# Performance work log

Hardware: AMD Instinct MI355X
Metric: run time of the kernel (lower is better)

The kernel has to match this reference:

```python
import jax, jax.numpy as jnp
import numpy as np

B, G, D, L, F = 64, 1024, 256, 2, 1024  # batch, graph_size, embed_dim, n_layers, ffn hidden
NEG = -30.0  # mask fill value when evaluate=False (training path)


def _uniform(key, shape, fan):
    stdv = 1.0 / np.sqrt(fan)
    return jax.random.uniform(key, shape, jnp.float32, -stdv, stdv)


def setup_inputs() -> dict:
    key = jax.random.key(0)
    ks = jax.random.split(key, 12)
    x = jax.random.normal(ks[0], (B, G, D), jnp.float32)
    mask = jax.random.randint(ks[1], (B, G), 0, 2, jnp.int32)  # 1 = attention blocked
    # weights stored as [in, out] (transposed vs torch Linear); same math.
    Wq = _uniform(ks[2], (L, D, D), D)
    Wk = _uniform(ks[3], (L, D, D), D)
    Wv = _uniform(ks[4], (L, D, D), D)
    Wo = _uniform(ks[5], (L, D, D), D)
    bo = _uniform(ks[6], (L, D), D)
    Wf1 = _uniform(ks[7], (L, D, F), D)
    bf1 = _uniform(ks[8], (L, F), F)
    Wf2 = _uniform(ks[9], (L, F, D), F)
    bf2 = _uniform(ks[10], (L, D), D)
    return {"x": x, "mask": mask, "Wq": Wq, "Wk": Wk, "Wv": Wv,
            "Wo": Wo, "bo": bo, "Wf1": Wf1, "bf1": bf1, "Wf2": Wf2, "bf2": bf2}


def reference(x, mask, Wq, Wk, Wv, Wo, bo, Wf1, bf1, Wf2, bf2):
    # GraphAttentionEncoder with n_heads=1 (key_dim = val_dim = embed_dim).
    m = mask.astype(bool)[:, None, :]            # [B,1,G] -> broadcast over query dim
    norm = 1.0 / jnp.sqrt(jnp.asarray(D, x.dtype))
    h = x
    for l in range(L):
        # --- MultiHeadAttention with residual (SkipConnection) ---
        q = h @ Wq[l]                            # [B,G,D]
        k = h @ Wk[l]
        v = h @ Wv[l]
        c = norm * jnp.einsum('bqd,bkd->bqk', q, k)   # [B,G,G]
        c = jnp.where(m, NEG, c)                 # masked fill (-30, evaluate=False)
        a = jax.nn.softmax(c, axis=-1)
        a = jnp.where(m, 0.0, a)                 # post-softmax zeroing of masked weights
        heads = jnp.einsum('bqk,bkd->bqd', a, v)
        h = h + heads @ Wo[l] + bo[l]
        # --- feed-forward with residual (SkipConnection_Linear) ---
        h = h + jax.nn.relu(h @ Wf1[l] + bf1[l]) @ Wf2[l] + bf2[l]
    return h, h.mean(axis=1)
```

## Files before the change

kernel.cpp:

```cpp
#include <hip/hip_runtime.h>
#include <hip/hip_bf16.h>

#define Bdim 64
#define Gdim 1024
#define Ddim 256
#define Fdim 1024

typedef short s8v __attribute__((ext_vector_type(8)));
typedef float f4v __attribute__((ext_vector_type(4)));

__device__ __forceinline__ float bf2f(short s){
  return __uint_as_float(((unsigned)(unsigned short)s) << 16);
}
__device__ __forceinline__ short f2bf(float f){
  unsigned u = __float_as_uint(f);
  u = u + 0x7fffu + ((u >> 16) & 1u);
  return (short)(u >> 16);
}
__device__ __forceinline__ s8v ld8(const short* p){ return *(const s8v*)p; }

#define MFMA_BF16(a,b,c) __builtin_amdgcn_mfma_f32_16x16x32_bf16((a),(b),(c),0,0,0)

#define GLDS16(gp, lp) __builtin_amdgcn_global_load_lds( \
    (const __attribute__((address_space(1))) void*)(gp), \
    (__attribute__((address_space(3))) void*)(lp), 16, 0, 0)

__global__ __launch_bounds__(256) void detect_dtype(const unsigned* __restrict__ x,
                                                    int* __restrict__ flag){
  __shared__ int cnt[256];
  int c = 0;
  #pragma unroll
  for (int j=0;j<4;j++){
    unsigned u = x[threadIdx.x*4 + j];
    int e = (u >> 7) & 0xFF;
    c += (e >= 100 && e <= 140) ? 1 : 0;
  }
  cnt[threadIdx.x] = c;
  __syncthreads();
  if (threadIdx.x == 0){
    int s = 0;
    for (int i=0;i<256;i++) s += cnt[i];
    flag[0] = (s >= 512) ? 0 : 1;
  }
}

__global__ void diag_ws(void* o, float v, const int* __restrict__ flag){
  if (threadIdx.x == 0){
    if (flag[0]){ ((float*)o)[0] = v; ((float*)o)[16777216] = v; }
    else        { ((short*)o)[0] = f2bf(v); ((short*)o)[16777216] = f2bf(v); }
  }
}

__global__ __launch_bounds__(256) void cast_in(const void* __restrict__ x,
                                               float* __restrict__ h32,
                                               const int* __restrict__ flag){
  size_t i = ((size_t)blockIdx.x * 256 + threadIdx.x) * 8;
  if (flag[0]){
    const float* xf = (const float*)x;
    #pragma unroll
    for (int j=0;j<8;j++) h32[i+j] = xf[i+j];
  } else {
    s8v v = ld8((const short*)x + i);
    #pragma unroll
    for (int j=0;j<8;j++) h32[i+j] = bf2f(v[j]);
  }
}

__global__ __launch_bounds__(256) void transpose_w(const void* __restrict__ src,
                                                   short* __restrict__ dh, int R, int C,
                                                   const int* __restrict__ flag,
                                                   int dzs, int dbase){
  __shared__ short th[32][33];
  int fl = flag[0];
  size_t soff = (size_t)blockIdx.z * R * C;
  size_t doff = (size_t)dbase + (size_t)blockIdx.z * dzs;
  int c0 = blockIdx.x*32, r0 = blockIdx.y*32;
  int tx = threadIdx.x, ty = threadIdx.y;
  #pragma unroll
  for (int i=ty;i<32;i+=8){
    size_t idx = soff + (size_t)(r0+i)*C + (c0+tx);
    float w = fl ? ((const float*)src)[idx] : bf2f(((const short*)src)[idx]);
    th[i][tx] = f2bf(w);
  }
  __syncthreads();
  #pragma unroll
  for (int i=ty;i<32;i+=8)
    dh[doff + (size_t)(c0+i)*R + (r0+tx)] = th[tx][i];
}

__global__ __launch_bounds__(256) void bias_prep(const void* __restrict__ bo,
                                                 const void* __restrict__ bf1,
                                                 const void* __restrict__ bf2,
                                                 float* __restrict__ biasf,
                                                 const int* __restrict__ flag){
  int fl = flag[0];
  int i = blockIdx.x*256 + threadIdx.x;
  const void* src; int idx;
  if (i < 512){ src = bo; idx = i; }
  else if (i < 2560){ src = bf1; idx = i - 512; }
  else { src = bf2; idx = i - 2560; }
  biasf[i] = fl ? ((const float*)src)[idx] : bf2f(((const short*)src)[idx]);
}

template<int AM, int EPI>
__global__ __launch_bounds__(256) void gemm_t(
    const void* __restrict__ Ap, const short* __restrict__ Bh,
    const float* __restrict__ bias, float* __restrict__ hout,
    short* __restrict__ outb, int N, int K, int lda, int ldb, int Mrows)
{
  constexpr int AT = (AM==2) ? 2 : 1;
  __shared__ short As[AT*128*40];
  __shared__ short Bs[128*40];
  short* Asl = As + 128*40;
  const int tid = threadIdx.x;
  const int lane = tid & 63, wave = tid >> 6;
  const int quad = lane >> 4, l16 = lane & 15;
  const int m0 = blockIdx.x * 128, n0 = blockIdx.y * 128;
  const int wr = wave >> 1, wc = wave & 1;
  f4v acc[4][4];
  #pragma unroll
  for (int i=0;i<4;i++)
    #pragma unroll
    for (int j=0;j<4;j++) acc[i][j] = f4v{0.f,0.f,0.f,0.f};

  for (int k0 = 0; k0 < K; k0 += 32){
    __syncthreads();
    #pragma unroll
    for (int i=0;i<2;i++){
      int v = tid + i*256;
      int r = v >> 2, c8 = (v & 3) * 8;
      if (AM == 0){
        *(s8v*)(&As[r*40 + c8]) = ld8((const short*)Ap + (size_t)(m0 + r)*lda + k0 + c8);
      } else {
        const float* af = (const float*)Ap + (size_t)(m0 + r)*lda + k0 + c8;
        float4 f0 = *(const float4*)af;
        float4 f1 = *(const float4*)(af + 4);
        float fv[8] = {f0.x,f0.y,f0.z,f0.w,f1.x,f1.y,f1.z,f1.w};
        s8v hi, lo;
        #pragma unroll
        for (int j=0;j<8;j++) hi[j] = f2bf(fv[j]);
        *(s8v*)(&As[r*40 + c8]) = hi;
        if (AM == 2){
          #pragma unroll
          for (int j=0;j<8;j++) lo[j] = f2bf(fv[j] - bf2f(hi[j]));
          *(s8v*)(&Asl[r*40 + c8]) = lo;
        }
      }
      *(s8v*)(&Bs[r*40 + c8]) = ld8(Bh + (size_t)(n0 + r)*ldb + k0 + c8);
    }
    __syncthreads();
    s8v ah[4], al[4], bh[4];
    #pragma unroll
    for (int t=0;t<4;t++){
      ah[t] = ld8(&As[(wr*64 + t*16 + l16)*40 + quad*8]);
      bh[t] = ld8(&Bs[(wc*64 + t*16 + l16)*40 + quad*8]);
      if (AM == 2) al[t] = ld8(&Asl[(wr*64 + t*16 + l16)*40 + quad*8]);
    }
    #pragma unroll
    for (int ti=0;ti<4;ti++)
      #pragma unroll
      for (int tj=0;tj<4;tj++){
        acc[ti][tj] = MFMA_BF16(ah[ti], bh[tj], acc[ti][tj]);
        if (AM == 2) acc[ti][tj] = MFMA_BF16(al[ti], bh[tj], acc[ti][tj]);
      }
  }
  #pragma unroll
  for (int tj=0;tj<4;tj++){
    int col = n0 + wc*64 + tj*16 + l16;
    float bs = (EPI==1 || EPI==4) ? (bias ? bias[col] : 0.f) : 0.f;
    #pragma unroll
    for (int ti=0;ti<4;ti++){
      #pragma unroll
      for (int r=0;r<4;r++){
        int row = m0 + wr*64 + ti*16 + quad*4 + r;
        float v = acc[ti][tj][r];
        if (EPI == 0){
          outb[(size_t)row * N + col] = f2bf(v);
        } else if (EPI == 1){
          v += bs; v = v > 0.f ? v : 0.f;
          outb[(size_t)row * N + col] = f2bf(v);
        } else if (EPI == 4){
          size_t idx = (size_t)row * N + col;
          hout[idx] += v + bs;
        } else {
          int sec = col >> 8, c = col & 255;
          if (sec == 0)      outb[(size_t)row*256 + c] = f2bf(v);
          else if (sec == 1) (outb + (size_t)Mrows*256)[(size_t)row*256 + c] = f2bf(v);
          else {
            int bb = row >> 10, g = row & 1023;
            (outb + (size_t)2*Mrows*256)[(size_t)bb*262144 + (size_t)c*1024 + g] = f2bf(v);
          }
        }
      }
    }
  }
}

__global__ __launch_bounds__(512, 2) void flash_attn(
    const short* __restrict__ Q, const short* __restrict__ Kmat,
    const short* __restrict__ Vt, const int* __restrict__ mask,
    short* __restrict__ H)
{
  __shared__ short Ks[2][64*256];
  __shared__ short Vs[2][256*64];
  __shared__ short Ps[8][16*72];
  const int tid = threadIdx.x;
  const int lane = tid & 63, wave = tid >> 6;
  const int quad = lane >> 4, l16 = lane & 15;
  const int bid = blockIdx.x;
  const int b  = (bid & 7) + ((bid >> 6) << 3);
  const int qt = (bid >> 3) & 7;
  const short* Qb  = Q    + (size_t)b*Gdim*Ddim;
  const short* Kb  = Kmat + (size_t)b*Gdim*Ddim;
  const short* Vtb = Vt   + (size_t)b*Ddim*Gdim;
  const int qbase = qt*128 + wave*16;

  auto stage = [&](int buf, int k0){
    #pragma unroll
    for (int i=0;i<4;i++){
      int idx = i*512 + tid;
      int r = idx >> 5, g = idx & 31;
      GLDS16(Kb + (size_t)(k0 + r)*Ddim + ((g ^ (r & 7)) << 3), &Ks[buf][idx*8]);
    }
    #pragma unroll
    for (int i=0;i<4;i++){
      int idx = i*512 + tid;
      int d = idx >> 3, g = idx & 7;
      GLDS16(Vtb + (size_t)d*Gdim + k0 + ((g ^ (d & 7)) << 3), &Vs[buf][idx*8]);
    }
  };

  s8v qf[8];
  #pragma unroll
  for (int s=0;s<8;s++)
    qf[s] = ld8(Qb + (size_t)(qbase + l16)*Ddim + s*32 + quad*8);
  float mrow[4], lsum[4];
  #pragma unroll
  for (int r=0;r<4;r++){ mrow[r] = -1e9f; lsum[r] = 0.f; }
  f4v O[16];
  #pragma unroll
  for (int t=0;t<16;t++) O[t] = f4v{0.f,0.f,0.f,0.f};
  short* Pw = Ps[wave];

  stage(0, 0);
  __syncthreads();
  int cur = 0;
  for (int kt=0; kt<16; kt++){
    const int k0 = kt*64;
    if (kt < 15) stage(cur^1, k0 + 64);
    int mk[4];
    #pragma unroll
    for (int tj=0;tj<4;tj++) mk[tj] = mask[b*Gdim + k0 + tj*16 + l16];
    f4v sc[4];
    #pragma unroll
    for (int tj=0;tj<4;tj++) sc[tj] = f4v{0.f,0.f,0.f,0.f};
    const short* Kc = &Ks[cur][0];
    __builtin_amdgcn_s_setprio(1);
    #pragma unroll
    for (int st=0; st<8; st++){
      #pragma unroll
      for (int tj=0;tj<4;tj++){
        int row = tj*16 + l16;
        s8v kb = ld8(Kc + row*256 + (((st*4 + quad) ^ (row & 7)) << 3));
        sc[tj] = MFMA_BF16(qf[st], kb, sc[tj]);
      }
    }
    __builtin_amdgcn_s_setprio(0);
    float al[4]; bool need = false;
    #pragma unroll
    for (int r=0;r<4;r++){
      float mx = -1e9f;
      #pragma unroll
      for (int tj=0;tj<4;tj++){
        float v = sc[tj][r] * 0.0625f;
        if (mk[tj]) v = -30.f;
        sc[tj][r] = v;
        mx = fmaxf(mx, v);
      }
      #pragma unroll
      for (int mm=1; mm<16; mm<<=1) mx = fmaxf(mx, __shfl_xor(mx, mm));
      float mn = fmaxf(mrow[r], mx);
      al[r] = __expf(mrow[r] - mn);
      need |= (al[r] < 1.f);
      mrow[r] = mn;
      float ps = 0.f;
      #pragma unroll
      for (int tj=0;tj<4;tj++){
        float e = __expf(sc[tj][r] - mn);
        ps += e;
        sc[tj][r] = mk[tj] ? 0.f : e;
      }
      lsum[r] = lsum[r]*al[r] + ps;
    }
    if (__any(need)){
      #pragma unroll
      for (int t=0;t<16;t++)
        #pragma unroll
        for (int r=0;r<4;r++) O[t][r] *= al[r];
    }
    #pragma unroll
    for (int tj=0;tj<4;tj++)
      #pragma unroll
      for (int r=0;r<4;r++)
        Pw[(quad*4 + r)*72 + tj*16 + l16] = f2bf(sc[tj][r]);
    asm volatile("s_waitcnt lgkmcnt(0)" ::: "memory");
    __builtin_amdgcn_sched_barrier(0);
    const short* Vc = &Vs[cur][0];
    __builtin_amdgcn_s_setprio(1);
    #pragma unroll
    for (int st=0; st<2; st++){
      s8v pa = ld8(&Pw[l16*72 + st*32 + quad*8]);
      #pragma unroll
      for (int tt=0; tt<16; tt++){
        int d = tt*16 + l16;
        s8v vb = ld8(Vc + d*64 + (((st*4 + quad) ^ (d & 7)) << 3));
        O[tt] = MFMA_BF16(pa, vb, O[tt]);
      }
    }
    __builtin_amdgcn_s_setprio(0);
    __syncthreads();
    cur ^= 1;
  }
  float dn[4];
  #pragma unroll
  for (int r=0;r<4;r++){
    float s = lsum[r];
    #pragma unroll
    for (int mm=1; mm<16; mm<<=1) s += __shfl_xor(s, mm);
    dn[r] = fmaxf(s, 1e-30f);
  }
  #pragma unroll
  for (int t=0;t<16;t++){
    #pragma unroll
    for (int r=0;r<4;r++){
      int row = qbase + quad*4 + r;
      int col = t*16 + l16;
      H[((size_t)b*Gdim + row)*Ddim + col] = f2bf(O[t][r] / dn[r]);
    }
  }
}

__global__ __launch_bounds__(256) void mean_partial(const float* __restrict__ h32,
                                                    float* __restrict__ part){
  int b = blockIdx.x, c = blockIdx.y, d = threadIdx.x;
  float s = 0.f;
  for (int g = c*64; g < c*64 + 64; g++)
    s += h32[((size_t)b*Gdim + g)*Ddim + d];
  part[(b*16 + c)*Ddim + d] = s;
}
__global__ __launch_bounds__(256) void mean_final_dyn(const float* __restrict__ part,
                                                      void* __restrict__ out,
                                                      const int* __restrict__ flag){
  int i = blockIdx.x*256 + threadIdx.x;
  int b = i >> 8, d = i & 255;
  float s = 0.f;
  #pragma unroll
  for (int c=0;c<16;c++) s += part[(b*16 + c)*Ddim + d];
  s *= (1.f/1024.f);
  if (flag[0]) ((float*)out)[16777216 + i] = s;
  else         ((short*)out)[16777216 + i] = f2bf(s);
}
__global__ __launch_bounds__(256) void store_h(const float* __restrict__ h32,
                                               void* __restrict__ out,
                                               const int* __restrict__ flag){
  size_t i = (size_t)blockIdx.x*256 + threadIdx.x;
  if (flag[0]) ((float*)out)[i] = h32[i];
  else         ((short*)out)[i] = f2bf(h32[i]);
}

extern "C" void kernel_launch(void* const* d_in, const int* in_sizes, int n_in,
                              void* d_out, int out_size, void* d_ws, size_t ws_size,
                              hipStream_t stream)
{
  const void* xs  = d_in[0];
  const int*  mask= (const int*)d_in[1];
  const void* Wq  = d_in[2];
  const void* Wk  = d_in[3];
  const void* Wv  = d_in[4];
  const void* Wo  = d_in[5];
  const void* bo  = d_in[6];
  const void* Wf1 = d_in[7];
  const void* bf1 = d_in[8];
  const void* Wf2 = d_in[9];
  const void* bf2 = d_in[10];

  const size_t W_ALL = 786432 + 262144 + 1048576 + 1048576 + 12288;
  const size_t BASE  = 256 + 67108864;
  int CB;
  if      (ws_size >= BASE + 134217728ull + W_ALL) CB = 64;
  else if (ws_size >= BASE +  67108864ull + W_ALL) CB = 32;
  else if (ws_size >= BASE +  33554432ull + W_ALL) CB = 16;
  else CB = 0;

  char* p = (char*)d_ws;
  int* flag = (int*)p; p += 256;
  detect_dtype<<<1, 256, 0, stream>>>((const unsigned*)xs, flag);
  if (CB == 0){
    diag_ws<<<1, 64, 0, stream>>>(d_out, 2000.f + (float)(ws_size >> 20), flag);
    return;
  }
  const int M = CB * 1024, nch = 64 / CB;
  float* h32 = (float*)p; p += 67108864;
  char* arena = p;        p += (size_t)CB * 2097152;
  short* WqkvT = (short*)p; p += 786432;
  short* WoT   = (short*)p; p += 262144;
  short* Wf1T  = (short*)p; p += 1048576;
  short* Wf2T  = (short*)p; p += 1048576;
  float* biasf = (float*)p; p += 12288;
  float* part  = (float*)arena;

  short* Qc  = (short*)arena;
  short* Kc  = Qc + (size_t)M*256;
  short* Vtc = Qc + (size_t)2*M*256;
  short* Hc  = Qc + (size_t)3*M*256;
  short* Tc  = Qc;

  cast_in<<<8192, 256, 0, stream>>>(xs, h32, flag);
  dim3 tb(32,8);
  transpose_w<<<dim3(8,8,2),  tb, 0, stream>>>(Wq,  WqkvT, 256, 256,  flag, 196608, 0);
  transpose_w<<<dim3(8,8,2),  tb, 0, stream>>>(Wk,  WqkvT, 256, 256,  flag, 196608, 65536);
  transpose_w<<<dim3(8,8,2),  tb, 0, stream>>>(Wv,  WqkvT, 256, 256,  flag, 196608, 131072);
  transpose_w<<<dim3(8,8,2),  tb, 0, stream>>>(Wo,  WoT,   256, 256,  flag, 65536, 0);
  transpose_w<<<dim3(32,8,2), tb, 0, stream>>>(Wf1, Wf1T,  256, 1024, flag, 262144, 0);
  transpose_w<<<dim3(8,32,2), tb, 0, stream>>>(Wf2, Wf2T,  1024, 256, flag, 262144, 0);
  bias_prep<<<12, 256, 0, stream>>>(bo, bf1, bf2, biasf, flag);

  for (int c=0; c<nch; c++){
    float* hc = h32 + (size_t)c*M*256;
    const int* mc = mask + (size_t)c*M;
    for (int l=0; l<2; l++){
      gemm_t<1,5><<<dim3(M/128,6), 256, 0, stream>>>(hc, WqkvT + l*196608, nullptr,
                                                     nullptr, Qc, 768, 256, 256, 256, M);
      flash_attn<<<dim3(8*CB), 512, 0, stream>>>(Qc, Kc, Vtc, mc, Hc);
      gemm_t<0,4><<<dim3(M/128,2), 256, 0, stream>>>(Hc, WoT + l*65536, biasf + l*256,
                                                     hc, nullptr, 256, 256, 256, 256, M);
      gemm_t<2,1><<<dim3(M/128,8), 256, 0, stream>>>(hc, Wf1T + l*262144, biasf + 512 + l*1024,
                                                     nullptr, Tc, 1024, 256, 256, 256, M);
      gemm_t<0,4><<<dim3(M/128,2), 256, 0, stream>>>(Tc, Wf2T + l*262144, biasf + 2560 + l*256,
                                                     hc, nullptr, 256, 1024, 1024, 1024, M);
    }
  }
  mean_partial<<<dim3(64,16), 256, 0, stream>>>(h32, part);
  store_h<<<65536, 256, 0, stream>>>(h32, d_out, flag);
  mean_final_dyn<<<64, 256, 0, stream>>>(part, d_out, flag);
}
```

Before: 1.196 ms.

## Transpose QK^T MFMA so each lane owns one query row in softmax

Swaps the MFMA operands so the score tile is transposed: each lane holds one query row across keys. The row max and sum then need only two cross-lane shuffles instead of a 16-lane butterfly per row. The mask becomes a single coalesced load plus a ballot, and P is written to LDS as packed 4-element vectors. Rescaling is lazy: the running max is updated and O rescaled only when some row's new max exceeds the old one by more than 8. Skipped rescales can let exponentials grow up to e^8, which adds some overflow and precision risk in exchange for fewer rescaling passes.

```diff
diff --git a/kernel.cpp b/kernel.cpp
--- a/kernel.cpp
+++ b/kernel.cpp
@@ -7,6 +7,7 @@
 #define Fdim 1024
 
 typedef short s8v __attribute__((ext_vector_type(8)));
+typedef short s4v __attribute__((ext_vector_type(4)));
 typedef float f4v __attribute__((ext_vector_type(4)));
 
 __device__ __forceinline__ float bf2f(short s){
@@ -234,9 +235,7 @@
   #pragma unroll
   for (int s=0;s<8;s++)
     qf[s] = ld8(Qb + (size_t)(qbase + l16)*Ddim + s*32 + quad*8);
-  float mrow[4], lsum[4];
-  #pragma unroll
-  for (int r=0;r<4;r++){ mrow[r] = -1e9f; lsum[r] = 0.f; }
+  float mrow = -1e9f, lsum = 0.f;
   f4v O[16];
   #pragma unroll
   for (int t=0;t<16;t++) O[t] = f4v{0.f,0.f,0.f,0.f};
@@ -248,9 +247,7 @@
   for (int kt=0; kt<16; kt++){
     const int k0 = kt*64;
     if (kt < 15) stage(cur^1, k0 + 64);
-    int mk[4];
-    #pragma unroll
-    for (int tj=0;tj<4;tj++) mk[tj] = mask[b*Gdim + k0 + tj*16 + l16];
+    int mv = mask[b*Gdim + k0 + lane];
     f4v sc[4];
     #pragma unroll
     for (int tj=0;tj<4;tj++) sc[tj] = f4v{0.f,0.f,0.f,0.f};
@@ -262,47 +259,52 @@
       for (int tj=0;tj<4;tj++){
         int row = tj*16 + l16;
         s8v kb = ld8(Kc + row*256 + (((st*4 + quad) ^ (row & 7)) << 3));
-        sc[tj] = MFMA_BF16(qf[st], kb, sc[tj]);
+        sc[tj] = MFMA_BF16(kb, qf[st], sc[tj]);
       }
     }
     __builtin_amdgcn_s_setprio(0);
-    float al[4]; bool need = false;
-    #pragma unroll
-    for (int r=0;r<4;r++){
-      float mx = -1e9f;
-      #pragma unroll
-      for (int tj=0;tj<4;tj++){
+    unsigned long long mb = __ballot(mv != 0);
+    float pm = -1e9f;
+    #pragma unroll
+    for (int tj=0;tj<4;tj++){
+      unsigned mb4 = (unsigned)(mb >> (tj*16 + quad*4)) & 15u;
+      #pragma unroll
+      for (int r=0;r<4;r++){
         float v = sc[tj][r] * 0.0625f;
-        if (mk[tj]) v = -30.f;
+        if ((mb4 >> r) & 1u) v = -30.f;
         sc[tj][r] = v;
-        mx = fmaxf(mx, v);
-      }
-      #pragma unroll
-      for (int mm=1; mm<16; mm<<=1) mx = fmaxf(mx, __shfl_xor(mx, mm));
-      float mn = fmaxf(mrow[r], mx);
-      al[r] = __expf(mrow[r] - mn);
-      need |= (al[r] < 1.f);
-      mrow[r] = mn;
-      float ps = 0.f;
-      #pragma unroll
-      for (int tj=0;tj<4;tj++){
-        float e = __expf(sc[tj][r] - mn);
-        ps += e;
-        sc[tj][r] = mk[tj] ? 0.f : e;
-      }
-      lsum[r] = lsum[r]*al[r] + ps;
-    }
-    if (__any(need)){
+        pm = fmaxf(pm, v);
+      }
+    }
+    pm = fmaxf(pm, __shfl_xor(pm, 16));
+    pm = fmaxf(pm, __shfl_xor(pm, 32));
+    if (!__all(pm <= mrow + 8.f)){
+      float mn = fmaxf(mrow, pm);
+      float al = __expf(mrow - mn);
+      mrow = mn;
+      lsum *= al;
+      float alr[4];
+      #pragma unroll
+      for (int r=0;r<4;r++) alr[r] = __shfl(al, quad*4 + r);
       #pragma unroll
       for (int t=0;t<16;t++)
         #pragma unroll
-        for (int r=0;r<4;r++) O[t][r] *= al[r];
-    }
-    #pragma unroll
-    for (int tj=0;tj<4;tj++)
-      #pragma unroll
-      for (int r=0;r<4;r++)
-        Pw[(quad*4 + r)*72 + tj*16 + l16] = f2bf(sc[tj][r]);
+        for (int r=0;r<4;r++) O[t][r] *= alr[r];
+    }
+    float ps = 0.f;
+    #pragma unroll
+    for (int tj=0;tj<4;tj++){
+      unsigned mb4 = (unsigned)(mb >> (tj*16 + quad*4)) & 15u;
+      s4v pk;
+      #pragma unroll
+      for (int r=0;r<4;r++){
+        float e = __expf(sc[tj][r] - mrow);
+        ps += e;
+        pk[r] = ((mb4 >> r) & 1u) ? (short)0 : f2bf(e);
+      }
+      *(s4v*)(&Pw[l16*72 + tj*16 + quad*4]) = pk;
+    }
+    lsum += ps;
     asm volatile("s_waitcnt lgkmcnt(0)" ::: "memory");
     __builtin_amdgcn_sched_barrier(0);
     const short* Vc = &Vs[cur][0];
@@ -321,21 +323,19 @@
     __syncthreads();
     cur ^= 1;
   }
-  float dn[4];
-  #pragma unroll
-  for (int r=0;r<4;r++){
-    float s = lsum[r];
-    #pragma unroll
-    for (int mm=1; mm<16; mm<<=1) s += __shfl_xor(s, mm);
-    dn[r] = fmaxf(s, 1e-30f);
-  }
+  float s = lsum;
+  s += __shfl_xor(s, 16);
+  s += __shfl_xor(s, 32);
+  float dnr[4];
+  #pragma unroll
+  for (int r=0;r<4;r++) dnr[r] = fmaxf(__shfl(s, quad*4 + r), 1e-30f);
   #pragma unroll
   for (int t=0;t<16;t++){
     #pragma unroll
     for (int r=0;r<4;r++){
       int row = qbase + quad*4 + r;
       int col = t*16 + l16;
-      H[((size_t)b*Gdim + row)*Ddim + col] = f2bf(O[t][r] / dn[r]);
+      H[((size_t)b*Gdim + row)*Ddim + col] = f2bf(O[t][r] / dnr[r]);
     }
   }
 }
```

Measured after the change: 1.176 ms. About the same (-1.7%).

## Double-buffer GEMM tiles with direct global-to-LDS loads and XOR swizzle

Applied to the files above, without the earlier changes.

Restructures the generic GEMM main loop to double-buffer LDS tiles. The next K-slice is prefetched while MFMAs run on the current one: via global_load_lds for bf16 operands, and via register prefetch plus deferred bf16 conversion for fp32 A. It drops the padded 40-stride layout in favour of a 32-stride XOR-swizzled layout so the direct-to-LDS writes stay contiguous and bank conflicts are avoided, and it raises wave priority around the MFMA block. This removes one barrier per iteration and hides global load latency. The cost is doubled LDS use and more registers for the fp32 prefetch path.

```diff
diff --git a/kernel.cpp b/kernel.cpp
--- a/kernel.cpp
+++ b/kernel.cpp
@@ -7,6 +7,7 @@
 #define Fdim 1024
 
 typedef short s8v __attribute__((ext_vector_type(8)));
+typedef short s4v __attribute__((ext_vector_type(4)));
 typedef float f4v __attribute__((ext_vector_type(4)));
 
 __device__ __forceinline__ float bf2f(short s){
@@ -108,54 +109,87 @@
     const float* __restrict__ bias, float* __restrict__ hout,
     short* __restrict__ outb, int N, int K, int lda, int ldb, int Mrows)
 {
-  constexpr int AT = (AM==2) ? 2 : 1;
-  __shared__ short As[AT*128*40];
-  __shared__ short Bs[128*40];
-  short* Asl = As + 128*40;
+  __shared__ short As[2][128*32];
+  __shared__ short Bs[2][128*32];
+  __shared__ short Asl[(AM==2)?2:1][(AM==2)?128*32:1];
   const int tid = threadIdx.x;
   const int lane = tid & 63, wave = tid >> 6;
   const int quad = lane >> 4, l16 = lane & 15;
   const int m0 = blockIdx.x * 128, n0 = blockIdx.y * 128;
   const int wr = wave >> 1, wc = wave & 1;
+  const int roff = ((quad ^ (l16 & 3)) << 3);
   f4v acc[4][4];
   #pragma unroll
   for (int i=0;i<4;i++)
     #pragma unroll
     for (int j=0;j<4;j++) acc[i][j] = f4v{0.f,0.f,0.f,0.f};
 
-  for (int k0 = 0; k0 < K; k0 += 32){
+  int rr[2], ss[2], dst[2];
+  #pragma unroll
+  for (int i=0;i<2;i++){
+    int idx = i*256 + tid;
+    rr[i] = idx >> 2;
+    ss[i] = (idx & 3) ^ (rr[i] & 3);
+    dst[i] = idx * 8;
+  }
+
+  auto stageB = [&](int buf, int k0){
+    #pragma unroll
+    for (int i=0;i<2;i++)
+      GLDS16(Bh + (size_t)(n0 + rr[i])*ldb + k0 + ss[i]*8, &Bs[buf][dst[i]]);
+  };
+  auto stageA0 = [&](int buf, int k0){
+    #pragma unroll
+    for (int i=0;i<2;i++)
+      GLDS16((const short*)Ap + (size_t)(m0 + rr[i])*lda + k0 + ss[i]*8, &As[buf][dst[i]]);
+  };
+
+  const int T = K >> 5;
+  int cur = 0;
+  float4 pf0a, pf0b, pf1a, pf1b;
+  stageB(0, 0);
+  if (AM == 0){
+    stageA0(0, 0);
+  } else {
+    #pragma unroll
+    for (int i=0;i<2;i++){
+      const float* ap = (const float*)Ap + (size_t)(m0 + rr[i])*lda + ss[i]*8;
+      float4 a = *(const float4*)ap, b = *(const float4*)(ap + 4);
+      float fv[8] = {a.x,a.y,a.z,a.w,b.x,b.y,b.z,b.w};
+      s8v hi, lo;
+      #pragma unroll
+      for (int j=0;j<8;j++) hi[j] = f2bf(fv[j]);
+      *(s8v*)(&As[0][dst[i]]) = hi;
+      if (AM == 2){
+        #pragma unroll
+        for (int j=0;j<8;j++) lo[j] = f2bf(fv[j] - bf2f(hi[j]));
+        *(s8v*)(&Asl[0][dst[i]]) = lo;
+      }
+    }
+  }
+
+  for (int t = 0; t < T; ++t){
     __syncthreads();
-    #pragma unroll
-    for (int i=0;i<2;i++){
-      int v = tid + i*256;
-      int r = v >> 2, c8 = (v & 3) * 8;
+    const int nk = (t + 1) << 5;
+    if (t + 1 < T){
+      stageB(cur ^ 1, nk);
       if (AM == 0){
-        *(s8v*)(&As[r*40 + c8]) = ld8((const short*)Ap + (size_t)(m0 + r)*lda + k0 + c8);
+        stageA0(cur ^ 1, nk);
       } else {
-        const float* af = (const float*)Ap + (size_t)(m0 + r)*lda + k0 + c8;
-        float4 f0 = *(const float4*)af;
-        float4 f1 = *(const float4*)(af + 4);
-        float fv[8] = {f0.x,f0.y,f0.z,f0.w,f1.x,f1.y,f1.z,f1.w};
-        s8v hi, lo;
-        #pragma unroll
-        for (int j=0;j<8;j++) hi[j] = f2bf(fv[j]);
-        *(s8v*)(&As[r*40 + c8]) = hi;
-        if (AM == 2){
-          #pragma unroll
-          for (int j=0;j<8;j++) lo[j] = f2bf(fv[j] - bf2f(hi[j]));
-          *(s8v*)(&Asl[r*40 + c8]) = lo;
-        }
-      }
-      *(s8v*)(&Bs[r*40 + c8]) = ld8(Bh + (size_t)(n0 + r)*ldb + k0 + c8);
-    }
-    __syncthreads();
+        const float* ap0 = (const float*)Ap + (size_t)(m0 + rr[0])*lda + nk + ss[0]*8;
+        const float* ap1 = (const float*)Ap + (size_t)(m0 + rr[1])*lda + nk + ss[1]*8;
+        pf0a = *(const float4*)ap0; pf0b = *(const float4*)(ap0 + 4);
+        pf1a = *(const float4*)ap1; pf1b = *(const float4*)(ap1 + 4);
+      }
+    }
     s8v ah[4], al[4], bh[4];
     #pragma unroll
-    for (int t=0;t<4;t++){
-      ah[t] = ld8(&As[(wr*64 + t*16 + l16)*40 + quad*8]);
-      bh[t] = ld8(&Bs[(wc*64 + t*16 + l16)*40 + quad*8]);
-      if (AM == 2) al[t] = ld8(&Asl[(wr*64 + t*16 + l16)*40 + quad*8]);
-    }
+    for (int q=0;q<4;q++){
+      ah[q] = ld8(&As[cur][(wr*64 + q*16 + l16)*32 + roff]);
+      bh[q] = ld8(&Bs[cur][(wc*64 + q*16 + l16)*32 + roff]);
+      if (AM == 2) al[q] = ld8(&Asl[cur][(wr*64 + q*16 + l16)*32 + roff]);
+    }
+    __builtin_amdgcn_s_setprio(1);
     #pragma unroll
     for (int ti=0;ti<4;ti++)
       #pragma unroll
@@ -163,6 +197,26 @@
         acc[ti][tj] = MFMA_BF16(ah[ti], bh[tj], acc[ti][tj]);
         if (AM == 2) acc[ti][tj] = MFMA_BF16(al[ti], bh[tj], acc[ti][tj]);
       }
+    __builtin_amdgcn_s_setprio(0);
+    if (AM != 0 && t + 1 < T){
+      float fv0[8] = {pf0a.x,pf0a.y,pf0a.z,pf0a.w,pf0b.x,pf0b.y,pf0b.z,pf0b.w};
+      float fv1[8] = {pf1a.x,pf1a.y,pf1a.z,pf1a.w,pf1b.x,pf1b.y,pf1b.z,pf1b.w};
+      s8v hi0, hi1, lo0, lo1;
+      #pragma unroll
+      for (int j=0;j<8;j++){ hi0[j] = f2bf(fv0[j]); hi1[j] = f2bf(fv1[j]); }
+      *(s8v*)(&As[cur^1][dst[0]]) = hi0;
+      *(s8v*)(&As[cur^1][dst[1]]) = hi1;
+      if (AM == 2){
+        #pragma unroll
+        for (int j=0;j<8;j++){
+          lo0[j] = f2bf(fv0[j] - bf2f(hi0[j]));
+          lo1[j] = f2bf(fv1[j] - bf2f(hi1[j]));
+        }
+        *(s8v*)(&Asl[cur^1][dst[0]]) = lo0;
+        *(s8v*)(&Asl[cur^1][dst[1]]) = lo1;
+      }
+    }
+    cur ^= 1;
   }
   #pragma unroll
   for (int tj=0;tj<4;tj++){
```

New measurement: 1.174 ms. No clear change (-1.8%).
